# Optimization experiments

Hardware: AMD Instinct MI355X
Metric: run time of the kernel (lower is better)

## Reference

```python
import jax, jax.numpy as jnp
import numpy as np
from jax import lax

STRIDE = 1
PADDING = 1


def setup_inputs() -> dict:
    key = jax.random.key(0)
    k1, k2 = jax.random.split(key)
    x = jax.random.normal(k1, (32, 128, 56, 56), dtype=jnp.float32)
    weight = jax.random.normal(k2, (256, 128, 3, 3), dtype=jnp.float32)
    bias = jnp.zeros((256,), dtype=jnp.float32)
    return {"x": x, "weight": weight, "bias": bias}


def reference(x, weight, bias):
    # Standard 2D cross-correlation (the intended math of the torch
    # unfold + broadcast-multiply + sum implementation):
    #   out[b,o,h,w] = sum_{i,kh,kw} x_pad[b,i,h*s+kh,w*s+kw] * weight[o,i,kh,kw] + bias[o]
    out = lax.conv_general_dilated(
        x, weight,
        window_strides=(STRIDE, STRIDE),
        padding=[(PADDING, PADDING), (PADDING, PADDING)],
        dimension_numbers=("NCHW", "OIHW", "NCHW"),
    )
    return out + bias[None, :, None, None]
```

## Files before the change

kernel.cpp:

```cpp
#include <hip/hip_runtime.h>
#include <cstdint>
#include <cstddef>

#define NB    32
#define CI    128
#define CO    256
#define HW_   56
#define HP    58
#define KTOT  1152
#define NKT   36
#define MTOT  (NB * HW_ * HW_)

static constexpr size_t XP_ELEMS = (size_t)NB * HP * HP * CI;
static constexpr size_t WT_ELEMS = (size_t)CO * KTOT;
static constexpr size_t XP_BYTES = XP_ELEMS * 2;
static constexpr size_t WT_BYTES = WT_ELEMS * 2;

typedef __attribute__((ext_vector_type(8))) short bf16x8;
typedef __attribute__((ext_vector_type(4))) float f32x4;

__device__ __forceinline__ short f32_to_bf16(float f) {
  uint32_t u = __float_as_uint(f);
  uint32_t r = (u + 0x7FFFu + ((u >> 16) & 1u)) >> 16;
  return (short)r;
}

typedef __attribute__((address_space(3))) void       lds_void;
typedef const __attribute__((address_space(1))) void gbl_void;

__device__ __forceinline__ void gload16(const void* g, void* l) {
  __builtin_amdgcn_global_load_lds((gbl_void*)g, (lds_void*)l, 16, 0, 0);
}

__global__ void pad_convert(const float* __restrict__ x, short* __restrict__ xp,
                            const float* __restrict__ wt, short* __restrict__ wbT) {
  __shared__ float lds[CI][57];
  const int blk = blockIdx.x;
  const int hp  = blk % HP;
  const int nb  = blk / HP;
  const int tid = threadIdx.x;

  if (blk < 1152) {
    int idx = blk * 256 + tid;
    int c  = idx & 127;
    int t  = idx >> 7;
    int kw = t % 3;  int t2 = t / 3;
    int kh = t2 % 3; int o  = t2 / 3;
    wbT[idx] = f32_to_bf16(wt[(((size_t)o * CI + c) * 3 + kh) * 3 + kw]);
  }

  const bool interior = (hp >= 1 && hp <= HW_);
  if (interior) {
    const float* src = x + (size_t)nb * CI * HW_ * HW_ + (size_t)(hp - 1) * HW_;
    for (int t = tid; t < CI * HW_; t += 256) {
      int c = t / HW_, w = t - (t / HW_) * HW_;
      lds[c][w] = src[(size_t)c * HW_ * HW_ + w];
    }
  }
  __syncthreads();
  short* dst = xp + (size_t)(nb * HP + hp) * HP * CI;
  for (int t = tid; t < HP * CI / 4; t += 256) {
    const int wp = t >> 5;
    const int c4 = (t & 31) * 4;
    short4 s;
    if (interior && wp >= 1 && wp <= HW_) {
      s.x = f32_to_bf16(lds[c4 + 0][wp - 1]);
      s.y = f32_to_bf16(lds[c4 + 1][wp - 1]);
      s.z = f32_to_bf16(lds[c4 + 2][wp - 1]);
      s.w = f32_to_bf16(lds[c4 + 3][wp - 1]);
    } else {
      s.x = s.y = s.z = s.w = 0;
    }
    *(short4*)(dst + t * 4) = s;
  }
}

__device__ __forceinline__ int stage_aoff(int u) {
  const int tap = u >> 2;
  const int cq  = u & 3;
  const int kh  = tap / 3, kw = tap - kh * 3;
  return ((kh * HP + kw) * CI + cq * 32) * 2;
}

__global__ __launch_bounds__(256, 3) void conv_gemm(
    const short* __restrict__ xp, const short* __restrict__ wbT,
    const float* __restrict__ bias, float* __restrict__ out) {
  __shared__ __align__(16) char lds_[3 * 16384];

  const int tid = threadIdx.x;
  const int l   = tid & 63;
  const int wv  = tid >> 6;
  const int wm  = wv >> 1;
  const int wn  = wv & 1;

  const int bid = blockIdx.x;
  const int lin = (bid & 7) * 196 + (bid >> 3);
  const int mt  = lin >> 1;
  const int nt  = lin & 1;

  const int pcs  = (((l & 3) ^ ((l >> 3) & 3)) << 4);
  const int srow = 16 * wv + (l >> 2);
  const char *aSrc0, *aSrc1;
  {
#pragma unroll
    for (int g = 0; g < 2; ++g) {
      int m  = mt * 128 + 64 * g + srow;
      int nb = m / 3136, hw = m - nb * 3136;
      int h = hw / HW_, w = hw - (hw / HW_) * HW_;
      const char* p = (const char*)xp + ((size_t)((nb * HP + h) * HP + w) * CI) * 2 + pcs;
      if (g == 0) aSrc0 = p; else aSrc1 = p;
    }
  }
  const char* bSrc0 = (const char*)wbT + (size_t)(nt * 128 +      srow) * KTOT * 2 + pcs;
  const char* bSrc1 = (const char*)wbT + (size_t)(nt * 128 + 64 + srow) * KTOT * 2 + pcs;

  const int lm   = l & 15;
  const int koff = (((l >> 4) ^ ((l >> 1) & 3)) << 4);
  const int raOff = (wm * 64 + lm) * 64 + koff;
  const int rbOff = (wn * 64 + lm) * 64 + koff;

  char* B0 = lds_;
  char* B1 = lds_ + 16384;
  char* B2 = lds_ + 32768;

#define STAGE(U, BUF)                                                        \
  {                                                                          \
    const int ao_ = stage_aoff(U);                                           \
    const int bo_ = (U) * 64;                                                \
    gload16(aSrc0 + ao_, (BUF) +         wv * 1024);                         \
    gload16(aSrc1 + ao_, (BUF) +  4096 + wv * 1024);                         \
    gload16(bSrc0 + bo_, (BUF) +  8192 + wv * 1024);                         \
    gload16(bSrc1 + bo_, (BUF) + 12288 + wv * 1024);                         \
  }

  f32x4 acc[4][4];
#pragma unroll
  for (int g = 0; g < 4; ++g)
#pragma unroll
    for (int h = 0; h < 4; ++h) acc[g][h] = {0.f, 0.f, 0.f, 0.f};

  STAGE(0, B0)
  STAGE(1, B1)
  asm volatile("s_waitcnt vmcnt(4)" ::: "memory");
  __builtin_amdgcn_s_barrier();
  __builtin_amdgcn_sched_barrier(0);

#define TILE_BODY(V, CUR, STG)                                               \
  {                                                                          \
    const int v_ = (V);                                                      \
    if (v_ + 2 < NKT) STAGE(v_ + 2, STG)                                     \
    bf16x8 af[4], bf[4];                                                     \
    _Pragma("unroll") for (int g = 0; g < 4; ++g)                            \
        af[g] = *(const bf16x8*)((CUR) + raOff + g * 1024);                  \
    _Pragma("unroll") for (int h = 0; h < 4; ++h)                            \
        bf[h] = *(const bf16x8*)((CUR) + 8192 + rbOff + h * 1024);           \
    __builtin_amdgcn_s_setprio(1);                                           \
    _Pragma("unroll") for (int g = 0; g < 4; ++g)                            \
      _Pragma("unroll") for (int h = 0; h < 4; ++h)                          \
        acc[g][h] = __builtin_amdgcn_mfma_f32_16x16x32_bf16(                 \
            bf[h], af[g], acc[g][h], 0, 0, 0);                               \
    __builtin_amdgcn_s_setprio(0);                                           \
    if (v_ < NKT - 1) {                                                      \
      if (v_ == NKT - 2) { asm volatile("s_waitcnt vmcnt(0)" ::: "memory"); }\
      else               { asm volatile("s_waitcnt vmcnt(4)" ::: "memory"); }\
      __builtin_amdgcn_s_barrier();                                          \
      __builtin_amdgcn_sched_barrier(0);                                     \
    }                                                                        \
  }

  for (int v3 = 0; v3 < NKT; v3 += 3) {
    TILE_BODY(v3 + 0, B0, B2)
    TILE_BODY(v3 + 1, B1, B0)
    TILE_BODY(v3 + 2, B2, B1)
  }
#undef TILE_BODY
#undef STAGE

  const int mBase = mt * 128 + wm * 64 + lm;
  const int ocB   = nt * 128 + wn * 64 + (l >> 4) * 4;
  float bv[4][4];
#pragma unroll
  for (int h = 0; h < 4; ++h)
#pragma unroll
    for (int j = 0; j < 4; ++j) bv[h][j] = bias[ocB + h * 16 + j];
#pragma unroll
  for (int g = 0; g < 4; ++g) {
    const int m  = mBase + g * 16;
    const int nb = m / 3136;
    const int hw = m - nb * 3136;
    float* op = out + (size_t)nb * CO * 3136 + hw;
#pragma unroll
    for (int h = 0; h < 4; ++h) {
      const int oc = ocB + h * 16;
#pragma unroll
      for (int j = 0; j < 4; ++j)
        op[(size_t)(oc + j) * 3136] = acc[g][h][j] + bv[h][j];
    }
  }
}

__global__ void conv_naive(const float* __restrict__ x, const float* __restrict__ wt,
                           const float* __restrict__ bias, float* __restrict__ out) {
  const int idx = blockIdx.x * 256 + threadIdx.x;
  if (idx >= NB * CO * 3136) return;
  const int w  = idx % HW_;
  const int h  = (idx / HW_) % HW_;
  const int oc = (idx / 3136) % CO;
  const int nb = idx / (3136 * CO);
  float s = bias[oc];
  for (int c = 0; c < CI; ++c)
    for (int kh = 0; kh < 3; ++kh) {
      const int ih = h + kh - 1;
      if (ih < 0 || ih >= HW_) continue;
      for (int kw = 0; kw < 3; ++kw) {
        const int iw = w + kw - 1;
        if (iw < 0 || iw >= HW_) continue;
        s += x[((size_t)(nb * CI + c) * HW_ + ih) * HW_ + iw] *
             wt[(((size_t)oc * CI + c) * 3 + kh) * 3 + kw];
      }
    }
  out[idx] = s;
}

extern "C" void kernel_launch(void* const* d_in, const int* in_sizes, int n_in,
                              void* d_out, int out_size, void* d_ws, size_t ws_size,
                              hipStream_t stream) {
  const float* x    = (const float*)d_in[0];
  const float* wt   = (const float*)d_in[1];
  const float* bias = (const float*)d_in[2];
  float* out        = (float*)d_out;

  if (ws_size < XP_BYTES + WT_BYTES) {
    conv_naive<<<(NB * CO * 3136 + 255) / 256, 256, 0, stream>>>(x, wt, bias, out);
    return;
  }

  short* xp  = (short*)d_ws;
  short* wbT = (short*)((char*)d_ws + XP_BYTES);

  pad_convert<<<NB * HP, 256, 0, stream>>>(x, xp, wt, wbT);
  conv_gemm<<<(MTOT / 128) * 2, 256, 0, stream>>>(xp, wbT, bias, out);
}
```

Before: 98.51 us.

## Restructure GEMM pipeline to four LDS buffers processing two k-tiles per barrier

```diff
diff --git a/kernel.cpp b/kernel.cpp
--- a/kernel.cpp
+++ b/kernel.cpp
@@ -82,10 +82,10 @@
   return ((kh * HP + kw) * CI + cq * 32) * 2;
 }
 
-__global__ __launch_bounds__(256, 3) void conv_gemm(
+__global__ __launch_bounds__(256, 2) void conv_gemm(
     const short* __restrict__ xp, const short* __restrict__ wbT,
     const float* __restrict__ bias, float* __restrict__ out) {
-  __shared__ __align__(16) char lds_[3 * 16384];
+  __shared__ __align__(16) char lds_[4 * 16384];
 
   const int tid = threadIdx.x;
   const int l   = tid & 63;
@@ -118,10 +118,6 @@
   const int koff = (((l >> 4) ^ ((l >> 1) & 3)) << 4);
   const int raOff = (wm * 64 + lm) * 64 + koff;
   const int rbOff = (wn * 64 + lm) * 64 + koff;
-
-  char* B0 = lds_;
-  char* B1 = lds_ + 16384;
-  char* B2 = lds_ + 32768;
 
 #define STAGE(U, BUF)                                                        \
   {                                                                          \
@@ -133,47 +129,51 @@
     gload16(bSrc1 + bo_, (BUF) + 12288 + wv * 1024);                         \
   }
 
-  f32x4 acc[4][4];
-#pragma unroll
-  for (int g = 0; g < 4; ++g)
-#pragma unroll
-    for (int h = 0; h < 4; ++h) acc[g][h] = {0.f, 0.f, 0.f, 0.f};
-
-  STAGE(0, B0)
-  STAGE(1, B1)
-  asm volatile("s_waitcnt vmcnt(4)" ::: "memory");
-  __builtin_amdgcn_s_barrier();
-  __builtin_amdgcn_sched_barrier(0);
-
-#define TILE_BODY(V, CUR, STG)                                               \
+#define COMPUTE(BUF)                                                         \
   {                                                                          \
-    const int v_ = (V);                                                      \
-    if (v_ + 2 < NKT) STAGE(v_ + 2, STG)                                     \
     bf16x8 af[4], bf[4];                                                     \
     _Pragma("unroll") for (int g = 0; g < 4; ++g)                            \
-        af[g] = *(const bf16x8*)((CUR) + raOff + g * 1024);                  \
+        af[g] = *(const bf16x8*)((BUF) + raOff + g * 1024);                  \
     _Pragma("unroll") for (int h = 0; h < 4; ++h)                            \
-        bf[h] = *(const bf16x8*)((CUR) + 8192 + rbOff + h * 1024);           \
+        bf[h] = *(const bf16x8*)((BUF) + 8192 + rbOff + h * 1024);           \
     __builtin_amdgcn_s_setprio(1);                                           \
     _Pragma("unroll") for (int g = 0; g < 4; ++g)                            \
       _Pragma("unroll") for (int h = 0; h < 4; ++h)                          \
         acc[g][h] = __builtin_amdgcn_mfma_f32_16x16x32_bf16(                 \
             bf[h], af[g], acc[g][h], 0, 0, 0);                               \
     __builtin_amdgcn_s_setprio(0);                                           \
-    if (v_ < NKT - 1) {                                                      \
-      if (v_ == NKT - 2) { asm volatile("s_waitcnt vmcnt(0)" ::: "memory"); }\
-      else               { asm volatile("s_waitcnt vmcnt(4)" ::: "memory"); }\
-      __builtin_amdgcn_s_barrier();                                          \
-      __builtin_amdgcn_sched_barrier(0);                                     \
-    }                                                                        \
-  }
-
-  for (int v3 = 0; v3 < NKT; v3 += 3) {
-    TILE_BODY(v3 + 0, B0, B2)
-    TILE_BODY(v3 + 1, B1, B0)
-    TILE_BODY(v3 + 2, B2, B1)
-  }
-#undef TILE_BODY
+  }
+
+  char* buf[4] = { lds_, lds_ + 16384, lds_ + 32768, lds_ + 49152 };
+
+  f32x4 acc[4][4];
+#pragma unroll
+  for (int g = 0; g < 4; ++g)
+#pragma unroll
+    for (int h = 0; h < 4; ++h) acc[g][h] = {0.f, 0.f, 0.f, 0.f};
+
+  STAGE(0, buf[0])
+  STAGE(1, buf[1])
+  asm volatile("s_waitcnt vmcnt(0)" ::: "memory");
+  __builtin_amdgcn_s_barrier();
+  __builtin_amdgcn_sched_barrier(0);
+
+#define BODY(U, S0, S1, C0, C1, LAST)                                        \
+  {                                                                          \
+    if (!(LAST)) { STAGE((U) + 2, S0) STAGE((U) + 3, S1) }                   \
+    COMPUTE(C0)                                                              \
+    COMPUTE(C1)                                                              \
+    asm volatile("s_waitcnt vmcnt(0)" ::: "memory");                         \
+    __builtin_amdgcn_s_barrier();                                            \
+    __builtin_amdgcn_sched_barrier(0);                                       \
+  }
+
+  for (int u = 0; u < NKT; u += 4) {
+    BODY(u,     buf[2], buf[3], buf[0], buf[1], false)
+    BODY(u + 2, buf[0], buf[1], buf[2], buf[3], (u + 2 == NKT - 2))
+  }
+#undef BODY
+#undef COMPUTE
 #undef STAGE
 
   const int mBase = mt * 128 + wm * 64 + lm;
```

Result: faster. 95.85 us (-2.7%).
